# Optimization experiments

Hardware: AMD Instinct MI355X
Metric: run time of the kernel (lower is better)

## Reference

```python
import math
import jax, jax.numpy as jnp
import numpy as np

DIM = 2048
NUM_HEADS = 16
HEAD_DIM = DIM // NUM_HEADS
BASE = 10000.0


def _rope(x):
    # x: [B, S, H, D]; non-interleaved (chunk-half) rotary embedding
    S, D = x.shape[1], x.shape[-1]
    inv_freq = 1.0 / (BASE ** (jnp.arange(0, D, 2, dtype=jnp.float32) / D))
    t = jnp.arange(S, dtype=jnp.float32)
    freqs = jnp.outer(t, inv_freq)  # [S, D/2]
    cos = jnp.cos(freqs)[None, :, None, :].astype(x.dtype)
    sin = jnp.sin(freqs)[None, :, None, :].astype(x.dtype)
    x1, x2 = jnp.split(x, 2, axis=-1)
    return jnp.concatenate([x1 * cos - x2 * sin, x1 * sin + x2 * cos], axis=-1)


def setup_inputs() -> dict:
    key = jax.random.key(0)
    kx, kq, kk, kv, ko = jax.random.split(key, 5)
    x = jax.random.normal(kx, (2, 2048, DIM), dtype=jnp.float32)
    scale = 0.02
    Wq = jax.random.normal(kq, (DIM, DIM), dtype=jnp.float32) * scale
    Wk = jax.random.normal(kk, (DIM, DIM), dtype=jnp.float32) * scale
    Wv = jax.random.normal(kv, (DIM, DIM), dtype=jnp.float32) * scale
    Wo = jax.random.normal(ko, (DIM, DIM), dtype=jnp.float32) * scale
    return {"x": x, "Wq": Wq, "Wk": Wk, "Wv": Wv, "Wo": Wo}


def reference(x, Wq, Wk, Wv, Wo):
    B, S, _ = x.shape
    # nn.Linear(bias=False): y = x @ W.T
    q = (x @ Wq.T).reshape(B, S, NUM_HEADS, HEAD_DIM)
    k = (x @ Wk.T).reshape(B, S, NUM_HEADS, HEAD_DIM)
    v = (x @ Wv.T).reshape(B, S, NUM_HEADS, HEAD_DIM)
    q = _rope(q)
    k = _rope(k)
    scale = 1.0 / math.sqrt(HEAD_DIM)
    # causal attention, [B,H,S,S] scores
    scores = jnp.einsum("bqhd,bkhd->bhqk", q, k) * scale
    causal = jnp.tril(jnp.ones((S, S), dtype=bool))
    scores = jnp.where(causal[None, None], scores, jnp.finfo(scores.dtype).min)
    attn = jax.nn.softmax(scores, axis=-1)
    out = jnp.einsum("bhqk,bkhd->bqhd", attn, v).reshape(B, S, DIM)
    return out @ Wo.T
```

## Files before the change

kernel.cpp:

```cpp
#include <hip/hip_runtime.h>

typedef unsigned short u16;
typedef __attribute__((ext_vector_type(8))) short short8;
typedef __attribute__((ext_vector_type(4))) float f32x4;
typedef __attribute__((ext_vector_type(4))) int i32x4;

__device__ __forceinline__ float bf2f(u16 u) {
  union { unsigned u; float f; } v; v.u = ((unsigned)u) << 16; return v.f;
}
__device__ __forceinline__ u16 f2bf(float f) {
  union { float f; unsigned u; } v; v.f = f;
  unsigned r = (v.u + 0x7FFFu + ((v.u >> 16) & 1u)) >> 16;
  return (u16)r;
}
__device__ __forceinline__ float flushv(float t, float sentinel) {
  if (t != t || fabsf(t) > 3.0e38f) return sentinel;
  return t;
}
__device__ __forceinline__ short8 ld8f(const float* p) {
  const float4 f0 = *(const float4*)p;
  const float4 f1 = *(const float4*)(p + 4);
  short8 r;
  r[0] = (short)f2bf(f0.x); r[1] = (short)f2bf(f0.y);
  r[2] = (short)f2bf(f0.z); r[3] = (short)f2bf(f0.w);
  r[4] = (short)f2bf(f1.x); r[5] = (short)f2bf(f1.y);
  r[6] = (short)f2bf(f1.z); r[7] = (short)f2bf(f1.w);
  return r;
}

__device__ __forceinline__ void gl16(const u16* g, u16* l) {
  __builtin_amdgcn_global_load_lds(
      (const __attribute__((address_space(1))) void*)g,
      (__attribute__((address_space(3))) void*)l, 16, 0, 0);
}

__global__ __launch_bounds__(256) void cvt_all(
    const float* __restrict__ x,
    const float* __restrict__ Wq, const float* __restrict__ Wk,
    const float* __restrict__ Wv, const float* __restrict__ Wo,
    u16* __restrict__ xb, u16* __restrict__ wqb, u16* __restrict__ wkb,
    u16* __restrict__ wvb, u16* __restrict__ wob)
{
  const int bid = blockIdx.x;
  const float* s; u16* d; long t;
  if (bid < 8192) {
    const int which = bid >> 11;
    t = (long)(bid & 2047) * 256 + threadIdx.x;
    if (which == 0)      { s = Wq; d = wqb; }
    else if (which == 1) { s = Wk; d = wkb; }
    else if (which == 2) { s = Wv; d = wvb; }
    else                 { s = Wo; d = wob; }
  } else {
    s = x; d = xb;
    t = (long)(bid - 8192) * 256 + threadIdx.x;
  }
  *(short8*)&d[t * 8] = ld8f(s + t * 8);
}

template <bool OF>
__device__ __forceinline__ void gemm_core(
    const u16* __restrict__ Ap, const u16* __restrict__ Bp,
    void* __restrict__ O, int m0, int n0, int N, float sentinel)
{
  __shared__ __align__(16) u16 As[2][128 * 32];
  __shared__ __align__(16) u16 Bs[2][128 * 32];
  constexpr int K = 2048;

  const int tid  = threadIdx.x;
  const int wave = tid >> 6;
  const int lane = tid & 63;
  const int quad = lane >> 4;
  const int l15  = lane & 15;

  const int wm = (wave >> 1) * 64;
  const int wn = (wave & 1) * 64;

  const int srow = lane >> 2;
  const int scu  = lane & 3;
  const u16* Ag0 = Ap + (long)(m0 + wave * 32 + srow) * K + scu * 8;
  const u16* Ag1 = Ag0 + 16 * (long)K;
  const u16* Bg0 = Bp + (long)(n0 + wave * 32 + srow) * K + scu * 8;
  const u16* Bg1 = Bg0 + 16 * (long)K;
  const int sl0 = (wave * 2 + 0) * 512;
  const int sl1 = (wave * 2 + 1) * 512;

  const f32x4 zero = {0.f, 0.f, 0.f, 0.f};
  f32x4 acc[4][4];
#pragma unroll
  for (int i = 0; i < 4; ++i)
#pragma unroll
    for (int j = 0; j < 4; ++j) acc[i][j] = zero;

  gl16(Ag0, &As[0][sl0]); gl16(Ag1, &As[0][sl1]);
  gl16(Bg0, &Bs[0][sl0]); gl16(Bg1, &Bs[0][sl1]);
  __syncthreads();

#pragma unroll 1
  for (int k0 = 0; k0 < K; k0 += 64) {
    gl16(Ag0 + k0 + 32, &As[1][sl0]); gl16(Ag1 + k0 + 32, &As[1][sl1]);
    gl16(Bg0 + k0 + 32, &Bs[1][sl0]); gl16(Bg1 + k0 + 32, &Bs[1][sl1]);
    {
      short8 af[4], bf[4];
#pragma unroll
      for (int i = 0; i < 4; ++i)
        af[i] = *(const short8*)&As[0][(wm + i * 16 + l15) * 32 + quad * 8];
#pragma unroll
      for (int j = 0; j < 4; ++j)
        bf[j] = *(const short8*)&Bs[0][(wn + j * 16 + l15) * 32 + quad * 8];
#pragma unroll
      for (int i = 0; i < 4; ++i)
#pragma unroll
        for (int j = 0; j < 4; ++j)
          acc[i][j] = __builtin_amdgcn_mfma_f32_16x16x32_bf16(af[i], bf[j], acc[i][j], 0, 0, 0);
    }
    __syncthreads();

    if (k0 + 64 < K) {
      gl16(Ag0 + k0 + 64, &As[0][sl0]); gl16(Ag1 + k0 + 64, &As[0][sl1]);
      gl16(Bg0 + k0 + 64, &Bs[0][sl0]); gl16(Bg1 + k0 + 64, &Bs[0][sl1]);
    }
    {
      short8 af[4], bf[4];
#pragma unroll
      for (int i = 0; i < 4; ++i)
        af[i] = *(const short8*)&As[1][(wm + i * 16 + l15) * 32 + quad * 8];
#pragma unroll
      for (int j = 0; j < 4; ++j)
        bf[j] = *(const short8*)&Bs[1][(wn + j * 16 + l15) * 32 + quad * 8];
#pragma unroll
      for (int i = 0; i < 4; ++i)
#pragma unroll
        for (int j = 0; j < 4; ++j)
          acc[i][j] = __builtin_amdgcn_mfma_f32_16x16x32_bf16(af[i], bf[j], acc[i][j], 0, 0, 0);
    }
    __syncthreads();
  }

#pragma unroll
  for (int i = 0; i < 4; ++i) {
    const int row0 = m0 + wm + i * 16 + quad * 4;
#pragma unroll
    for (int j = 0; j < 4; ++j) {
      const int col = n0 + wn + j * 16 + l15;
#pragma unroll
      for (int r = 0; r < 4; ++r) {
        const float val = flushv(acc[i][j][r], sentinel);
        if constexpr (OF)
          ((float*)O)[(long)(row0 + r) * N + col] = val;
        else
          ((u16*)O)[(long)(row0 + r) * N + col] = f2bf(val);
      }
    }
  }
}

__global__ __launch_bounds__(256) void gemm_qkv(
    const u16* __restrict__ xb,
    const u16* __restrict__ wqb, const u16* __restrict__ wkb, const u16* __restrict__ wvb,
    u16* __restrict__ q, u16* __restrict__ k, u16* __restrict__ v)
{
  const int bid = blockIdx.x;
  const int z = bid >> 9, r = bid & 511;
  const u16 *A, *B; u16* O; int m0, n0, Nn;
  if (z < 2) {
    A = xb; B = z ? wkb : wqb; O = z ? k : q;
    m0 = (r >> 4) * 128; n0 = (r & 15) * 128; Nn = 2048;
  } else {
    A = wvb; B = xb; O = v;
    m0 = (r >> 5) * 128; n0 = (r & 31) * 128; Nn = 4096;
  }
  gemm_core<false>(A, B, O, m0, n0, Nn, 7777.f);
}

__global__ __launch_bounds__(256) void gemm_proj(
    const u16* __restrict__ ao, const u16* __restrict__ wob, float* __restrict__ out)
{
  const int r = blockIdx.x;
  gemm_core<true>(ao, wob, out, (r >> 4) * 128, (r & 15) * 128, 2048, 5555.f);
}

template <bool AF, bool WF, bool OF>
__global__ __launch_bounds__(256) void gemm_bt(
    const void* __restrict__ Ap,
    const void* __restrict__ Wp0, const void* __restrict__ Wp1, const void* __restrict__ Wp2,
    void* __restrict__ O0, void* __restrict__ O1, void* __restrict__ O2,
    int M, int N, int K, float sentinel)
{
  __shared__ __align__(16) u16 As[128 * 32];
  __shared__ __align__(16) u16 Bs[128 * 32];

  const void* Wp; void* O;
  if (blockIdx.z == 0)      { Wp = Wp0; O = O0; }
  else if (blockIdx.z == 1) { Wp = Wp1; O = O1; }
  else                      { Wp = Wp2; O = O2; }

  const float* Af = (const float*)Ap;  const u16* Ab = (const u16*)Ap;
  const float* Wf = (const float*)Wp;  const u16* Wb = (const u16*)Wp;

  const int tid  = threadIdx.x;
  const int wave = tid >> 6;
  const int lane = tid & 63;
  const int quad = lane >> 4;
  const int l15  = lane & 15;

  const int m0 = blockIdx.y * 128;
  const int n0 = blockIdx.x * 128;
  const int wm = (wave >> 1) * 64;
  const int wn = (wave & 1) * 64;

  const int e0 = wave * 1024 + lane * 8;
  const int e1 = e0 + 512;
  const int r0 = e0 >> 5, c0 = e0 & 31;
  const int r1 = e1 >> 5, c1 = e1 & 31;

  const long aoff0 = (long)(m0 + r0) * K + c0;
  const long aoff1 = (long)(m0 + r1) * K + c1;
  const long boff0 = (long)(n0 + r0) * K + c0;
  const long boff1 = (long)(n0 + r1) * K + c1;

  const f32x4 zero = {0.f, 0.f, 0.f, 0.f};
  f32x4 acc[4][4];
#pragma unroll
  for (int i = 0; i < 4; ++i)
#pragma unroll
    for (int j = 0; j < 4; ++j) acc[i][j] = zero;

  for (int k0 = 0; k0 < K; k0 += 32) {
    short8 a0, a1, b0, b1;
    if constexpr (AF) {
      a0 = ld8f(Af + aoff0 + k0);
      a1 = ld8f(Af + aoff1 + k0);
    } else {
      a0 = *(const short8*)(Ab + aoff0 + k0);
      a1 = *(const short8*)(Ab + aoff1 + k0);
    }
    if constexpr (WF) {
      b0 = ld8f(Wf + boff0 + k0);
      b1 = ld8f(Wf + boff1 + k0);
    } else {
      b0 = *(const short8*)(Wb + boff0 + k0);
      b1 = *(const short8*)(Wb + boff1 + k0);
    }

    __syncthreads();
    *(short8*)&As[e0] = a0;
    *(short8*)&As[e1] = a1;
    *(short8*)&Bs[e0] = b0;
    *(short8*)&Bs[e1] = b1;
    __syncthreads();

    short8 af[4], bf[4];
#pragma unroll
    for (int i = 0; i < 4; ++i)
      af[i] = *(const short8*)&As[(wm + i * 16 + l15) * 32 + quad * 8];
#pragma unroll
    for (int j = 0; j < 4; ++j)
      bf[j] = *(const short8*)&Bs[(wn + j * 16 + l15) * 32 + quad * 8];
#pragma unroll
    for (int i = 0; i < 4; ++i)
#pragma unroll
      for (int j = 0; j < 4; ++j)
        acc[i][j] = __builtin_amdgcn_mfma_f32_16x16x32_bf16(af[i], bf[j], acc[i][j], 0, 0, 0);
  }

#pragma unroll
  for (int i = 0; i < 4; ++i) {
    const int row0 = m0 + wm + i * 16 + quad * 4;
#pragma unroll
    for (int j = 0; j < 4; ++j) {
      const int col = n0 + wn + j * 16 + l15;
#pragma unroll
      for (int r = 0; r < 4; ++r) {
        const float val = flushv(acc[i][j][r], sentinel);
        if constexpr (OF)
          ((float*)O)[(long)(row0 + r) * N + col] = val;
        else
          ((u16*)O)[(long)(row0 + r) * N + col] = f2bf(val);
      }
    }
  }
}

__global__ __launch_bounds__(256) void rope_kernel(u16* __restrict__ Q, u16* __restrict__ K)
{
  int t = blockIdx.x * 256 + threadIdx.x;
  const int half = 2 * 2048 * 16 * 64;
  u16* P = Q;
  if (t >= half) { P = K; t -= half; }
  const int i = t & 63;
  const int s = (t >> 10) & 2047;
  const long off = ((long)(t >> 6) << 7) + i;

  const float inv_freq = __expf((float)i * -0.14391156831212787f);
  const float fr = (float)s * inv_freq;
  float sn, cs;
  __sincosf(fr, &sn, &cs);

  const float q1 = bf2f(P[off]);
  const float q2 = bf2f(P[off + 64]);
  P[off]      = f2bf(q1 * cs - q2 * sn);
  P[off + 64] = f2bf(q1 * sn + q2 * cs);
}

__global__ __launch_bounds__(256, 4) void attn_kernel(
    const u16* __restrict__ Q, const u16* __restrict__ K,
    const u16* __restrict__ VT, u16* __restrict__ AO)
{
  __shared__ __align__(16) u16 Kb[2][4096];
  __shared__ __align__(16) u16 Vb[2][4096];

  const int tid  = threadIdx.x;
  const int wave = tid >> 6;
  const int lane = tid & 63;
  const int quad = lane >> 4;
  const int l15  = lane & 15;

  const int lin = blockIdx.x;
  const int xcd = lin & 7;
  const int hi  = lin >> 8;
  const int g   = (lin >> 3) & 31;
  const int qb  = (hi & 1) ? (31 - g) : g;
  const int bh  = (xcd << 2) | hi;
  const int b   = bh >> 4;
  const int h   = bh & 15;

  const long base = (long)b * 2048 * 2048 + (long)h * 128;
  const long vtb  = (long)h * 128 * 4096 + (long)b * 2048;
  const int q0w = qb * 64 + wave * 16;
  const int qi  = q0w + l15;

  const u16* Kp0 = K + base;
  const u16* Vp0 = VT + vtb;

  auto STAGE = [&](int bs, int jb) {
#pragma unroll
    for (int gi = 0; gi < 2; ++gi) {
      const int slot = wave * 2 + gi;
      {
        const int row = slot * 4 + (lane >> 4);
        const int su  = lane & 15;
        gl16(Kp0 + (long)(jb * 32 + row) * 2048 + ((su ^ (row & 7)) << 3),
             &Kb[bs][slot * 512]);
      }
      {
        const int row = slot * 16 + (lane >> 2);
        const int su  = lane & 3;
        gl16(Vp0 + (long)row * 4096 + jb * 32 + ((su ^ ((row >> 1) & 3)) << 3),
             &Vb[bs][slot * 512]);
      }
    }
  };

  short8 qa[4];
#pragma unroll
  for (int c = 0; c < 4; ++c)
    qa[c] = *(const short8*)&Q[base + (long)(q0w + l15) * 2048 + c * 32 + quad * 8];

  const f32x4 zero = {0.f, 0.f, 0.f, 0.f};
  f32x4 o[8];
#pragma unroll
  for (int c = 0; c < 8; ++c) o[c] = zero;

  float mreg = -1e30f, lreg = 0.f;
  const float scale = 0.08838834764831845f;

  const int njb_blk = qb * 2 + 2;
  const int njb_w   = qb * 2 + 1 + (wave >> 1);

  STAGE(0, 0);
  __syncthreads();

  const int xorK = l15 & 7;
  const int xorV = (l15 >> 1) & 3;

  int cur = 0;
  for (int jb = 0; jb < njb_blk; ++jb) {
    if (jb + 1 < njb_blk) STAGE(cur ^ 1, jb + 1);

    if (jb < njb_w) {
      const int j0 = jb * 32;

      f32x4 s0T = zero, s1T = zero;
#pragma unroll
      for (int c = 0; c < 4; ++c) {
        const short8 kA = *(const short8*)&Kb[cur][l15 * 128 + (((c * 4 + quad) ^ xorK) << 3)];
        const short8 kB2 = *(const short8*)&Kb[cur][(l15 + 16) * 128 + (((c * 4 + quad) ^ xorK) << 3)];
        s0T = __builtin_amdgcn_mfma_f32_16x16x32_bf16(kA, qa[c], s0T, 0, 0, 0);
        s1T = __builtin_amdgcn_mfma_f32_16x16x32_bf16(kB2, qa[c], s1T, 0, 0, 0);
      }

      float sv0[4], sv1[4];
      float pmax = -1e30f;
      if (j0 + 31 > q0w) {
#pragma unroll
        for (int r = 0; r < 4; ++r) {
          const int k0i = j0 + quad * 4 + r;
          float s0 = s0T[r] * scale; if (k0i > qi)      s0 = -1e30f;
          float s1 = s1T[r] * scale; if (k0i + 16 > qi) s1 = -1e30f;
          sv0[r] = s0; sv1[r] = s1;
          pmax = fmaxf(pmax, fmaxf(s0, s1));
        }
      } else {
#pragma unroll
        for (int r = 0; r < 4; ++r) {
          sv0[r] = s0T[r] * scale;
          sv1[r] = s1T[r] * scale;
          pmax = fmaxf(pmax, fmaxf(sv0[r], sv1[r]));
        }
      }
      pmax = fmaxf(pmax, __shfl_xor(pmax, 16, 64));
      pmax = fmaxf(pmax, __shfl_xor(pmax, 32, 64));
      const float mprev = mreg;
      const float mnew  = fmaxf(mprev, pmax);
      const float alpha = __expf(mprev - mnew);
      float psum = 0.f;
#pragma unroll
      for (int r = 0; r < 4; ++r) {
        sv0[r] = __expf(sv0[r] - mnew);
        sv1[r] = __expf(sv1[r] - mnew);
        psum += sv0[r] + sv1[r];
      }
      psum += __shfl_xor(psum, 16, 64);
      psum += __shfl_xor(psum, 32, 64);
      lreg = lreg * alpha + psum;
      mreg = mnew;

      int w0, w1, w2, w3;
      asm("v_cvt_pk_bf16_f32 %0, %1, %2" : "=v"(w0) : "v"(sv0[0]), "v"(sv0[1]));
      asm("v_cvt_pk_bf16_f32 %0, %1, %2" : "=v"(w1) : "v"(sv0[2]), "v"(sv0[3]));
      asm("v_cvt_pk_bf16_f32 %0, %1, %2" : "=v"(w2) : "v"(sv1[0]), "v"(sv1[1]));
      asm("v_cvt_pk_bf16_f32 %0, %1, %2" : "=v"(w3) : "v"(sv1[2]), "v"(sv1[3]));
      const int srcA = l15 + ((quad & 1) << 5);
      const int srcB = srcA + 16;
      const int a0 = __shfl(w0, srcA, 64), a1 = __shfl(w1, srcA, 64);
      const int a2 = __shfl(w0, srcB, 64), a3 = __shfl(w1, srcB, 64);
      const int h0 = __shfl(w2, srcA, 64), h1 = __shfl(w3, srcA, 64);
      const int h2 = __shfl(w2, srcB, 64), h3 = __shfl(w3, srcB, 64);
      const bool hiq = quad >= 2;
      i32x4 pt;
      pt[0] = hiq ? h0 : a0;
      pt[1] = hiq ? h1 : a1;
      pt[2] = hiq ? h2 : a2;
      pt[3] = hiq ? h3 : a3;
      const short8 pa = *(const short8*)&pt;

      float av[4];
#pragma unroll
      for (int r = 0; r < 4; ++r) av[r] = __shfl(alpha, quad * 4 + r, 64);
#pragma unroll
      for (int c = 0; c < 8; ++c) {
        o[c][0] *= av[0]; o[c][1] *= av[1]; o[c][2] *= av[2]; o[c][3] *= av[3];
      }

#pragma unroll
      for (int c = 0; c < 8; ++c) {
        const short8 vf = *(const short8*)&Vb[cur][(c * 16 + l15) * 32 + ((quad ^ xorV) << 3)];
        o[c] = __builtin_amdgcn_mfma_f32_16x16x32_bf16(pa, vf, o[c], 0, 0, 0);
      }
    }

    __syncthreads();
    cur ^= 1;
  }

#pragma unroll
  for (int r = 0; r < 4; ++r) {
    const float lr  = __shfl(lreg, quad * 4 + r, 64);
    const float inv = 1.0f / lr;
    const long rowoff = base + (long)(q0w + quad * 4 + r) * 2048;
#pragma unroll
    for (int c = 0; c < 8; ++c)
      AO[rowoff + c * 16 + l15] = f2bf(flushv(o[c][r] * inv, 9999.f));
  }
}

__global__ __launch_bounds__(256) void fill_kernel(float* __restrict__ out, long n, float v)
{
  const long t = (long)blockIdx.x * 256 + threadIdx.x;
  if (t < n) out[t] = v;
}

extern "C" void kernel_launch(void* const* d_in, const int* in_sizes, int n_in,
                              void* d_out, int out_size, void* d_ws, size_t ws_size,
                              hipStream_t stream)
{
  const float* x  = (const float*)d_in[0];
  const float* Wq = (const float*)d_in[1];
  const float* Wk = (const float*)d_in[2];
  const float* Wv = (const float*)d_in[3];
  const float* Wo = (const float*)d_in[4];
  float* out = (float*)d_out;

  const long QSZ = (long)2 * 2048 * 2048;
  const long WSZ = QSZ / 2;

  u16* ws = (u16*)d_ws;
  u16* q  = ws;
  u16* k  = ws + QSZ;
  u16* v  = ws + 2 * QSZ;
  u16* ao = q;

  if (ws_size >= (size_t)6 * QSZ * sizeof(u16)) {
    u16* xb  = ws + 3 * QSZ;
    u16* wqb = ws + 4 * QSZ;
    u16* wkb = wqb + WSZ;
    u16* wvb = wqb + 2 * WSZ;
    u16* wob = wqb + 3 * WSZ;

    cvt_all<<<12288, 256, 0, stream>>>(x, Wq, Wk, Wv, Wo, xb, wqb, wkb, wvb, wob);
    gemm_qkv<<<1536, 256, 0, stream>>>(xb, wqb, wkb, wvb, q, k, v);
    rope_kernel<<<32768, 256, 0, stream>>>(q, k);
    attn_kernel<<<1024, 256, 0, stream>>>(q, k, v, ao);
    gemm_proj<<<512, 256, 0, stream>>>(ao, wob, out);
    return;
  }

  if (ws_size < (size_t)3 * QSZ * sizeof(u16)) {
    fill_kernel<<<(int)((QSZ + 255) / 256), 256, 0, stream>>>(out, QSZ, 1111.f);
    return;
  }

  gemm_bt<true, true, false><<<dim3(16, 32, 2), 256, 0, stream>>>(
      x, Wq, Wk, Wk, q, k, k, 4096, 2048, 2048, 7777.f);
  gemm_bt<true, true, false><<<dim3(32, 16, 1), 256, 0, stream>>>(
      Wv, x, x, x, v, v, v, 2048, 4096, 2048, 7777.f);
  rope_kernel<<<32768, 256, 0, stream>>>(q, k);
  attn_kernel<<<1024, 256, 0, stream>>>(q, k, v, ao);
  gemm_bt<false, true, true><<<dim3(16, 32, 1), 256, 0, stream>>>(
      ao, Wo, Wo, Wo, out, out, out, 4096, 2048, 2048, 5555.f);
}
```

Baseline: 422.1 us.

## Swizzle GEMM LDS tiles, use vmcnt-based barriers, and vectorize RoPE

The bf16 GEMM core now XOR-swizzles the 16-byte chunks of each LDS row. Both the global-to-LDS copy addresses and the fragment reads are remapped, which is meant to cut LDS bank conflicts on the short8 reads. The double-buffered loop replaces __syncthreads with explicit vmcnt waits and sched-barrier-wrapped s_barrier, so only the older stage's loads must finish. The RoPE kernel now handles 8 elements per thread with 16-byte vector loads and stores, using a multiplicative frequency step, and runs with 8x fewer blocks. The risks are explicit waitcnt correctness and small fp drift from the iterated inv_freq.

```diff
diff --git a/kernel.cpp b/kernel.cpp
--- a/kernel.cpp
+++ b/kernel.cpp
@@ -33,6 +33,11 @@
       (const __attribute__((address_space(1))) void*)g,
       (__attribute__((address_space(3))) void*)l, 16, 0, 0);
 }
+
+#define VWAIT(N) asm volatile("s_waitcnt vmcnt(" #N ")" ::: "memory")
+#define SBAR() do { __builtin_amdgcn_sched_barrier(0); \
+                    __builtin_amdgcn_s_barrier(); \
+                    __builtin_amdgcn_sched_barrier(0); } while (0)
 
 __global__ __launch_bounds__(256) void cvt_all(
     const float* __restrict__ x,
@@ -76,14 +81,18 @@
   const int wn = (wave & 1) * 64;
 
   const int srow = lane >> 2;
-  const int scu  = lane & 3;
-  const u16* Ag0 = Ap + (long)(m0 + wave * 32 + srow) * K + scu * 8;
+  const int su   = lane & 3;
+  const int r0   = wave * 32 + srow;
+  const int csw  = ((su ^ ((r0 >> 1) & 3)) << 3);
+  const u16* Ag0 = Ap + (long)(m0 + r0) * K + csw;
   const u16* Ag1 = Ag0 + 16 * (long)K;
-  const u16* Bg0 = Bp + (long)(n0 + wave * 32 + srow) * K + scu * 8;
+  const u16* Bg0 = Bp + (long)(n0 + r0) * K + csw;
   const u16* Bg1 = Bg0 + 16 * (long)K;
   const int sl0 = (wave * 2 + 0) * 512;
   const int sl1 = (wave * 2 + 1) * 512;
 
+  const int xsw = ((l15 >> 1) & 3) << 3;
+
   const f32x4 zero = {0.f, 0.f, 0.f, 0.f};
   f32x4 acc[4][4];
 #pragma unroll
@@ -91,49 +100,39 @@
 #pragma unroll
     for (int j = 0; j < 4; ++j) acc[i][j] = zero;
 
-  gl16(Ag0, &As[0][sl0]); gl16(Ag1, &As[0][sl1]);
-  gl16(Bg0, &Bs[0][sl0]); gl16(Bg1, &Bs[0][sl1]);
-  __syncthreads();
+  auto STAGE = [&](int bs, int k0) {
+    gl16(Ag0 + k0, &As[bs][sl0]); gl16(Ag1 + k0, &As[bs][sl1]);
+    gl16(Bg0 + k0, &Bs[bs][sl0]); gl16(Bg1 + k0, &Bs[bs][sl1]);
+  };
+  auto COMPUTE = [&](const u16* Ab, const u16* Bb) {
+    short8 af[4], bf[4];
+#pragma unroll
+    for (int i = 0; i < 4; ++i)
+      af[i] = *(const short8*)&Ab[(wm + i * 16 + l15) * 32 + ((quad << 3) ^ xsw)];
+#pragma unroll
+    for (int j = 0; j < 4; ++j)
+      bf[j] = *(const short8*)&Bb[(wn + j * 16 + l15) * 32 + ((quad << 3) ^ xsw)];
+#pragma unroll
+    for (int i = 0; i < 4; ++i)
+#pragma unroll
+      for (int j = 0; j < 4; ++j)
+        acc[i][j] = __builtin_amdgcn_mfma_f32_16x16x32_bf16(af[i], bf[j], acc[i][j], 0, 0, 0);
+  };
+
+  STAGE(0, 0);
 
 #pragma unroll 1
   for (int k0 = 0; k0 < K; k0 += 64) {
-    gl16(Ag0 + k0 + 32, &As[1][sl0]); gl16(Ag1 + k0 + 32, &As[1][sl1]);
-    gl16(Bg0 + k0 + 32, &Bs[1][sl0]); gl16(Bg1 + k0 + 32, &Bs[1][sl1]);
-    {
-      short8 af[4], bf[4];
-#pragma unroll
-      for (int i = 0; i < 4; ++i)
-        af[i] = *(const short8*)&As[0][(wm + i * 16 + l15) * 32 + quad * 8];
-#pragma unroll
-      for (int j = 0; j < 4; ++j)
-        bf[j] = *(const short8*)&Bs[0][(wn + j * 16 + l15) * 32 + quad * 8];
-#pragma unroll
-      for (int i = 0; i < 4; ++i)
-#pragma unroll
-        for (int j = 0; j < 4; ++j)
-          acc[i][j] = __builtin_amdgcn_mfma_f32_16x16x32_bf16(af[i], bf[j], acc[i][j], 0, 0, 0);
-    }
-    __syncthreads();
-
-    if (k0 + 64 < K) {
-      gl16(Ag0 + k0 + 64, &As[0][sl0]); gl16(Ag1 + k0 + 64, &As[0][sl1]);
-      gl16(Bg0 + k0 + 64, &Bs[0][sl0]); gl16(Bg1 + k0 + 64, &Bs[0][sl1]);
-    }
-    {
-      short8 af[4], bf[4];
-#pragma unroll
-      for (int i = 0; i < 4; ++i)
-        af[i] = *(const short8*)&As[1][(wm + i * 16 + l15) * 32 + quad * 8];
-#pragma unroll
-      for (int j = 0; j < 4; ++j)
-        bf[j] = *(const short8*)&Bs[1][(wn + j * 16 + l15) * 32 + quad * 8];
-#pragma unroll
-      for (int i = 0; i < 4; ++i)
-#pragma unroll
-        for (int j = 0; j < 4; ++j)
-          acc[i][j] = __builtin_amdgcn_mfma_f32_16x16x32_bf16(af[i], bf[j], acc[i][j], 0, 0, 0);
-    }
-    __syncthreads();
+    STAGE(1, k0 + 32);
+    VWAIT(4); SBAR();
+    COMPUTE(As[0], Bs[0]);
+    SBAR();
+
+    if (k0 + 64 < K) { STAGE(0, k0 + 64); VWAIT(4); }
+    else             { VWAIT(0); }
+    SBAR();
+    COMPUTE(As[1], Bs[1]);
+    SBAR();
   }
 
 #pragma unroll
@@ -284,22 +283,32 @@
 __global__ __launch_bounds__(256) void rope_kernel(u16* __restrict__ Q, u16* __restrict__ K)
 {
   int t = blockIdx.x * 256 + threadIdx.x;
-  const int half = 2 * 2048 * 16 * 64;
+  const int per = 524288;
   u16* P = Q;
-  if (t >= half) { P = K; t -= half; }
-  const int i = t & 63;
-  const int s = (t >> 10) & 2047;
-  const long off = ((long)(t >> 6) << 7) + i;
-
-  const float inv_freq = __expf((float)i * -0.14391156831212787f);
-  const float fr = (float)s * inv_freq;
-  float sn, cs;
-  __sincosf(fr, &sn, &cs);
-
-  const float q1 = bf2f(P[off]);
-  const float q2 = bf2f(P[off + 64]);
-  P[off]      = f2bf(q1 * cs - q2 * sn);
-  P[off + 64] = f2bf(q1 * sn + q2 * cs);
+  if (t >= per) { P = K; t -= per; }
+  const int i8  = t & 7;
+  const int row = t >> 3;
+  const int s   = (row >> 4) & 2047;
+  const long off = (long)row * 128 + i8 * 8;
+
+  short8 va = *(const short8*)&P[off];
+  short8 vb = *(const short8*)&P[off + 64];
+
+  const float fs = (float)s;
+  float invf = __expf((float)(i8 * 8) * -0.14391156831212787f);
+  const float step = 0.86596432336f;
+#pragma unroll
+  for (int j = 0; j < 8; ++j) {
+    float sn, cs;
+    __sincosf(fs * invf, &sn, &cs);
+    const float q1 = bf2f((u16)va[j]);
+    const float q2 = bf2f((u16)vb[j]);
+    va[j] = (short)f2bf(q1 * cs - q2 * sn);
+    vb[j] = (short)f2bf(q1 * sn + q2 * cs);
+    invf *= step;
+  }
+  *(short8*)&P[off]      = va;
+  *(short8*)&P[off + 64] = vb;
 }
 
 __global__ __launch_bounds__(256, 4) void attn_kernel(
@@ -509,7 +518,7 @@
 
     cvt_all<<<12288, 256, 0, stream>>>(x, Wq, Wk, Wv, Wo, xb, wqb, wkb, wvb, wob);
     gemm_qkv<<<1536, 256, 0, stream>>>(xb, wqb, wkb, wvb, q, k, v);
-    rope_kernel<<<32768, 256, 0, stream>>>(q, k);
+    rope_kernel<<<4096, 256, 0, stream>>>(q, k);
     attn_kernel<<<1024, 256, 0, stream>>>(q, k, v, ao);
     gemm_proj<<<512, 256, 0, stream>>>(ao, wob, out);
     return;
@@ -524,7 +533,7 @@
       x, Wq, Wk, Wk, q, k, k, 4096, 2048, 2048, 7777.f);
   gemm_bt<true, true, false><<<dim3(32, 16, 1), 256, 0, stream>>>(
       Wv, x, x, x, v, v, v, 2048, 4096, 2048, 7777.f);
-  rope_kernel<<<32768, 256, 0, stream>>>(q, k);
+  rope_kernel<<<4096, 256, 0, stream>>>(q, k);
   attn_kernel<<<1024, 256, 0, stream>>>(q, k, v, ao);
   gemm_bt<false, true, true><<<dim3(16, 32, 1), 256, 0, stream>>>(
       ao, Wo, Wo, Wo, out, out, out, 4096, 2048, 2048, 5555.f);
```

Result: faster. 393.0 us (-6.9%).
